# Kernel tuning notes

Hardware: AMD Instinct MI355X
Metric: run time of the kernel (lower is better)

The kernel has to match this reference:

```python
import jax, jax.numpy as jnp
import numpy as np

N = 50000      # nodes
E = 800000     # edges (avg degree 16)
DIN = 128
DH = 128
DOUT = 40
ALPHA = 0.1
BETA = 1.0


def gcn_conv(x, src, dst, ew, W, b, n):
    """PyG GCNConv: add self-loops, symmetric deg^-1/2 normalization, gather-scatter."""
    idx = jnp.arange(n)
    s = jnp.concatenate([src, idx])
    d = jnp.concatenate([dst, idx])
    w = jnp.concatenate([ew, jnp.ones((n,), x.dtype)])
    deg = jax.ops.segment_sum(w, d, num_segments=n)            # [N]
    dinv = jnp.where(deg > 0, jax.lax.rsqrt(deg), 0.0)
    norm = dinv[s] * w * dinv[d]                               # [E+N]
    h = x @ W                                                  # [N, dout]
    msg = h[s] * norm[:, None]                                 # gather + scale
    out = jax.ops.segment_sum(msg, d, num_segments=n)          # scatter-add
    return out + b


def setup_inputs() -> dict:
    key = jax.random.key(0)
    ks = jax.random.split(key, 10)
    x = jax.random.normal(ks[0], (N, DIN), jnp.float32)
    edge_index = jax.random.randint(ks[1], (2, E), 0, N, dtype=jnp.int64)
    edge_weight = jax.random.uniform(ks[2], (E,), jnp.float32)
    W1 = jax.random.normal(ks[3], (DIN, DH), jnp.float32) / np.float32(np.sqrt(DIN))
    b1 = jnp.zeros((DH,), jnp.float32)
    W2 = jax.random.normal(ks[4], (DH, DH), jnp.float32) / np.float32(np.sqrt(DH))
    b2 = jnp.zeros((DH,), jnp.float32)
    W3 = jax.random.normal(ks[5], (DH, DOUT), jnp.float32) / np.float32(np.sqrt(DH))
    b3 = jnp.zeros((DOUT,), jnp.float32)
    return {"x": x, "edge_index": edge_index, "edge_weight": edge_weight,
            "W1": W1, "b1": b1, "W2": W2, "b2": b2, "W3": W3, "b3": b3}


def reference(x, edge_index, edge_weight, W1, b1, W2, b2, W3, b3):
    src, dst = edge_index[0], edge_index[1]
    ones_w = jnp.ones((E,), x.dtype)
    h1 = jax.nn.relu(gcn_conv(x, src, dst, ones_w, W1, b1, N))   # conv1 (edge_weight=None)
    hc = gcn_conv(h1, src, dst, edge_weight, W2, b2, N)          # crf_layer with edge_weight
    h = ALPHA * h1 + BETA * hc                                   # weighted residual combo
    # LearnableBernoulliDropout: identity in eval mode
    out = gcn_conv(h, src, dst, ones_w, W3, b3, N)               # conv2
    return jax.nn.log_softmax(out, axis=1)
```

## Files before the change

### kernel.cpp

```cpp
#include <hip/hip_runtime.h>
#include <math.h>

#define DIN  128
#define DH   128
#define DOUT 40
#define ALPHA_C 0.1f
#define BETA_C  1.0f
#define SLOT 64

#define NPB 512
#define NPB_SHIFT 9
#define MAXBK 128
#define BCAP 12288

typedef __attribute__((ext_vector_type(8))) short short8;
typedef __attribute__((ext_vector_type(4))) float floatx4;

static inline int cdiv_h(int a, int b) { return (a + b - 1) / b; }

static __device__ __forceinline__ unsigned short f2b(float f) {
    unsigned u = __float_as_uint(f);
    u = u + 0x7FFFu + ((u >> 16) & 1u);
    return (unsigned short)(u >> 16);
}
static __device__ __forceinline__ unsigned pk2(float x, float y) {
    return (unsigned)f2b(x) | ((unsigned)f2b(y) << 16);
}
static __device__ __forceinline__ float2 b2f2(unsigned u) {
    float2 r;
    r.x = __uint_as_float(u << 16);
    r.y = __uint_as_float(u & 0xFFFF0000u);
    return r;
}
static __device__ __forceinline__ float b2f1(unsigned short u) {
    return __uint_as_float(((unsigned)u) << 16);
}

__global__ __launch_bounds__(256) void init_gcur(int* __restrict__ gcur, int nbk) {
    int b = threadIdx.x;
    if (b < nbk) gcur[b] = b * BCAP;
}

__global__ __launch_bounds__(256) void bucket_p1(const int* __restrict__ src,
                                                 const int* __restrict__ dst,
                                                 const float* __restrict__ ew,
                                                 int* __restrict__ gcur,
                                                 int2* __restrict__ stage,
                                                 int E, int nbk) {
    __shared__ int hist[MAXBK], off[MAXBK], sbase[MAXBK];
    int t = threadIdx.x;
    int nb = gridDim.x;
    int C = (E + nb - 1) / nb;
    int e0 = blockIdx.x * C;
    int e1 = e0 + C; if (e1 > E) e1 = E;

    for (int i = t; i < nbk; i += 256) { hist[i] = 0; off[i] = 0; }
    __syncthreads();
    for (int e = e0 + t; e < e1; e += 256)
        atomicAdd(&hist[dst[e] >> NPB_SHIFT], 1);
    __syncthreads();
    for (int i = t; i < nbk; i += 256)
        sbase[i] = atomicAdd(&gcur[i], hist[i]);
    __syncthreads();
    for (int e = e0 + t; e < e1; e += 256) {
        int d = dst[e];
        int b = d >> NPB_SHIFT;
        int pos = atomicAdd(&off[b], 1);
        int idx = sbase[b] + pos;
        if (idx < (b + 1) * BCAP) {
            int2 v;
            v.x = (src[e] & 0xFFFF) | ((d & (NPB - 1)) << 16);
            v.y = __float_as_int(ew[e]);
            stage[idx] = v;
        }
    }
}

__global__ __launch_bounds__(256) void bucket_p2(const int2* __restrict__ stage,
                                                 const int* __restrict__ gcur,
                                                 int2* __restrict__ csr,
                                                 int* __restrict__ cnt,
                                                 float* __restrict__ dinv1,
                                                 float* __restrict__ dinv2, int Nn) {
    __shared__ int   lcnt[NPB];
    __shared__ float lws[NPB];
    int b = blockIdx.x;
    int t = threadIdx.x;
    for (int i = t; i < NPB; i += 256) { lcnt[i] = 0; lws[i] = 0.f; }
    __syncthreads();

    int base = b * BCAP;
    int n = gcur[b] - base; if (n > BCAP) n = BCAP;
    for (int i = t; i < n; i += 256) {
        int2 v = stage[base + i];
        int dl = (v.x >> 16) & (NPB - 1);
        int pos = atomicAdd(&lcnt[dl], 1);
        atomicAdd(&lws[dl], __int_as_float(v.y));
        if (pos < SLOT) {
            int d = (b << NPB_SHIFT) + dl;
            int2 o; o.x = v.x & 0xFFFF; o.y = v.y;
            csr[(d << 6) + pos] = o;
        }
    }
    __syncthreads();

    int d0 = b << NPB_SHIFT;
    for (int i = t; i < NPB; i += 256) {
        int d = d0 + i;
        if (d < Nn) {
            int c = lcnt[i]; if (c > SLOT) c = SLOT;
            cnt[d] = c;
            dinv1[d] = rsqrtf((float)c + 1.f);
            dinv2[d] = rsqrtf(1.f + lws[i]);
        }
    }
}

template <bool ABF16>
__global__ __launch_bounds__(256) void gemm128(const void* __restrict__ Ain,
                                               const float* __restrict__ W,
                                               unsigned short* __restrict__ C, int M) {
    __shared__ short As[128 * 128];
    __shared__ short Bs[128 * 128];
    int t = threadIdx.x;
    int blockM = blockIdx.x * 128;

    {
        int r = t >> 1, h = t & 1;
        int rg = blockM + r; if (rg > M - 1) rg = M - 1;
        if (ABF16) {
            const uint4* arow = (const uint4*)((const unsigned short*)Ain + (size_t)rg * 128);
            #pragma unroll
            for (int i = 0; i < 8; ++i) {
                int chunk = h * 8 + i;
                uint4 v = arow[chunk];
                *(uint4*)&As[r * 128 + ((chunk ^ (r & 7)) * 8)] = v;
            }
        } else {
            const float4* arow = (const float4*)((const float*)Ain + (size_t)rg * 128);
            #pragma unroll
            for (int i = 0; i < 8; ++i) {
                int chunk = h * 8 + i;
                float4 v0 = arow[chunk * 2], v1 = arow[chunk * 2 + 1];
                uint4 p;
                p.x = pk2(v0.x, v0.y); p.y = pk2(v0.z, v0.w);
                p.z = pk2(v1.x, v1.y); p.w = pk2(v1.z, v1.w);
                *(uint4*)&As[r * 128 + ((chunk ^ (r & 7)) * 8)] = p;
            }
        }
    }
    {
        int n = t & 127;
        int k0 = (t >> 7) * 64;
        #pragma unroll
        for (int it = 0; it < 8; ++it) {
            int k = k0 + it * 8;
            float f0 = W[(size_t)(k + 0) * 128 + n];
            float f1 = W[(size_t)(k + 1) * 128 + n];
            float f2 = W[(size_t)(k + 2) * 128 + n];
            float f3 = W[(size_t)(k + 3) * 128 + n];
            float f4 = W[(size_t)(k + 4) * 128 + n];
            float f5 = W[(size_t)(k + 5) * 128 + n];
            float f6 = W[(size_t)(k + 6) * 128 + n];
            float f7 = W[(size_t)(k + 7) * 128 + n];
            uint4 p;
            p.x = pk2(f0, f1); p.y = pk2(f2, f3);
            p.z = pk2(f4, f5); p.w = pk2(f6, f7);
            *(uint4*)&Bs[n * 128 + (((k >> 3) ^ (n & 7)) * 8)] = p;
        }
    }
    __syncthreads();

    int w = t >> 6, l = t & 63;
    int q = l >> 4, lm = l & 15;
    int rowoff = (w >> 1) * 64, coloff = (w & 1) * 64;

    floatx4 acc[4][4] = {};
    #pragma unroll
    for (int ks = 0; ks < 4; ++ks) {
        int chunk = ks * 4 + q;
        int sw = (chunk ^ (lm & 7)) * 8;
        short8 af[4], bf[4];
        #pragma unroll
        for (int tm = 0; tm < 4; ++tm)
            af[tm] = *(const short8*)&As[(rowoff + tm * 16 + lm) * 128 + sw];
        #pragma unroll
        for (int tn = 0; tn < 4; ++tn)
            bf[tn] = *(const short8*)&Bs[(coloff + tn * 16 + lm) * 128 + sw];
        #pragma unroll
        for (int tm = 0; tm < 4; ++tm)
            #pragma unroll
            for (int tn = 0; tn < 4; ++tn)
                acc[tm][tn] = __builtin_amdgcn_mfma_f32_16x16x32_bf16(af[tm], bf[tn], acc[tm][tn], 0, 0, 0);
    }

    #pragma unroll
    for (int tm = 0; tm < 4; ++tm) {
        #pragma unroll
        for (int reg = 0; reg < 4; ++reg) {
            int row = blockM + rowoff + tm * 16 + q * 4 + reg;
            if (row >= M) continue;
            #pragma unroll
            for (int tn = 0; tn < 4; ++tn) {
                int col = coloff + tn * 16 + lm;
                C[(size_t)row * 128 + col] = f2b(acc[tm][tn][reg]);
            }
        }
    }
}

__global__ __launch_bounds__(256) void gemm40(const unsigned short* __restrict__ Ain,
                                              const float* __restrict__ W,
                                              unsigned short* __restrict__ Cb, int M) {
    __shared__ short As[128 * 128];
    __shared__ short Bs[48 * 128];
    int t = threadIdx.x;
    int blockM = blockIdx.x * 128;

    {
        int r = t >> 1, h = t & 1;
        int rg = blockM + r; if (rg > M - 1) rg = M - 1;
        const uint4* arow = (const uint4*)(Ain + (size_t)rg * 128);
        #pragma unroll
        for (int i = 0; i < 8; ++i) {
            int chunk = h * 8 + i;
            uint4 v = arow[chunk];
            *(uint4*)&As[r * 128 + ((chunk ^ (r & 7)) * 8)] = v;
        }
    }
    {
        int n = t & 63;
        int k0 = (t >> 6) * 32;
        #pragma unroll
        for (int it = 0; it < 4; ++it) {
            int k = k0 + it * 8;
            uint4 p = {0, 0, 0, 0};
            if (n < 40) {
                float f0 = W[(size_t)(k + 0) * 40 + n];
                float f1 = W[(size_t)(k + 1) * 40 + n];
                float f2 = W[(size_t)(k + 2) * 40 + n];
                float f3 = W[(size_t)(k + 3) * 40 + n];
                float f4 = W[(size_t)(k + 4) * 40 + n];
                float f5 = W[(size_t)(k + 5) * 40 + n];
                float f6 = W[(size_t)(k + 6) * 40 + n];
                float f7 = W[(size_t)(k + 7) * 40 + n];
                p.x = pk2(f0, f1); p.y = pk2(f2, f3);
                p.z = pk2(f4, f5); p.w = pk2(f6, f7);
            }
            if (n < 48)
                *(uint4*)&Bs[n * 128 + (((k >> 3) ^ (n & 7)) * 8)] = p;
        }
    }
    __syncthreads();

    int w = t >> 6, l = t & 63;
    int q = l >> 4, lm = l & 15;
    int rowoff = w * 32;

    floatx4 acc[2][3] = {};
    #pragma unroll
    for (int ks = 0; ks < 4; ++ks) {
        int chunk = ks * 4 + q;
        int sw = (chunk ^ (lm & 7)) * 8;
        short8 af[2], bf[3];
        #pragma unroll
        for (int tm = 0; tm < 2; ++tm)
            af[tm] = *(const short8*)&As[(rowoff + tm * 16 + lm) * 128 + sw];
        #pragma unroll
        for (int tn = 0; tn < 3; ++tn)
            bf[tn] = *(const short8*)&Bs[(tn * 16 + lm) * 128 + sw];
        #pragma unroll
        for (int tm = 0; tm < 2; ++tm)
            #pragma unroll
            for (int tn = 0; tn < 3; ++tn)
                acc[tm][tn] = __builtin_amdgcn_mfma_f32_16x16x32_bf16(af[tm], bf[tn], acc[tm][tn], 0, 0, 0);
    }

    #pragma unroll
    for (int tm = 0; tm < 2; ++tm) {
        #pragma unroll
        for (int reg = 0; reg < 4; ++reg) {
            int row = blockM + rowoff + tm * 16 + q * 4 + reg;
            if (row >= M) continue;
            Cb[(size_t)row * 40 + lm]      = f2b(acc[tm][0][reg]);
            Cb[(size_t)row * 40 + 16 + lm] = f2b(acc[tm][1][reg]);
            if (lm < 8)
                Cb[(size_t)row * 40 + 32 + lm] = f2b(acc[tm][2][reg]);
        }
    }
}

template <int MODE>
__global__ __launch_bounds__(256) void agg128(const unsigned short* __restrict__ hpre,
                                              unsigned short* __restrict__ io,
                                              const float* __restrict__ bias,
                                              const float* __restrict__ dinv,
                                              const int* __restrict__ cnt,
                                              const int2* __restrict__ csr, int n) {
    int row = blockIdx.x * 4 + (threadIdx.x >> 6);
    if (row >= n) return;
    int lane = threadIdx.x & 63;
    const unsigned* hp = (const unsigned*)hpre;

    float di = dinv[row];
    float d2 = di * di;
    float2 acc = b2f2(hp[(size_t)row * 64 + lane]);
    {
        float2 bb = ((const float2*)bias)[lane];
        acc.x = fmaf(acc.x, d2, bb.x);
        acc.y = fmaf(acc.y, d2, bb.y);
    }

    int c = cnt[row]; if (c > SLOT) c = SLOT;
    int jb = row << 6;
    int je = jb + c;
    int j = jb;

    while (j + 8 <= je) {
        int2 ee[8]; float2 ff[8];
        #pragma unroll
        for (int u = 0; u < 8; ++u) ee[u] = csr[j + u];
        #pragma unroll
        for (int u = 0; u < 8; ++u) ff[u] = b2f2(hp[(size_t)ee[u].x * 64 + lane]);
        #pragma unroll
        for (int u = 0; u < 8; ++u) {
            float cc = (MODE == 1) ? dinv[ee[u].x] * __int_as_float(ee[u].y) * di
                                   : dinv[ee[u].x] * di;
            acc.x = fmaf(cc, ff[u].x, acc.x);
            acc.y = fmaf(cc, ff[u].y, acc.y);
        }
        j += 8;
    }
    if (j + 4 <= je) {
        int2 ee[4]; float2 ff[4];
        #pragma unroll
        for (int u = 0; u < 4; ++u) ee[u] = csr[j + u];
        #pragma unroll
        for (int u = 0; u < 4; ++u) ff[u] = b2f2(hp[(size_t)ee[u].x * 64 + lane]);
        #pragma unroll
        for (int u = 0; u < 4; ++u) {
            float cc = (MODE == 1) ? dinv[ee[u].x] * __int_as_float(ee[u].y) * di
                                   : dinv[ee[u].x] * di;
            acc.x = fmaf(cc, ff[u].x, acc.x);
            acc.y = fmaf(cc, ff[u].y, acc.y);
        }
        j += 4;
    }
    for (; j < je; ++j) {
        int2 e0 = csr[j];
        float cc = (MODE == 1) ? dinv[e0.x] * __int_as_float(e0.y) * di
                               : dinv[e0.x] * di;
        float2 f0 = b2f2(hp[(size_t)e0.x * 64 + lane]);
        acc.x = fmaf(cc, f0.x, acc.x);
        acc.y = fmaf(cc, f0.y, acc.y);
    }

    unsigned* iop = (unsigned*)io;
    if (MODE == 0) {
        acc.x = fmaxf(acc.x, 0.f); acc.y = fmaxf(acc.y, 0.f);
        iop[(size_t)row * 64 + lane] = pk2(acc.x, acc.y);
    } else {
        float2 h1 = b2f2(iop[(size_t)row * 64 + lane]);
        acc.x = fmaf(ALPHA_C, h1.x, BETA_C * acc.x);
        acc.y = fmaf(ALPHA_C, h1.y, BETA_C * acc.y);
        iop[(size_t)row * 64 + lane] = pk2(acc.x, acc.y);
    }
}

__global__ __launch_bounds__(256) void agg40_lsm(const unsigned short* __restrict__ h40,
                                                 const float* __restrict__ bias,
                                                 const float* __restrict__ dinv,
                                                 const int* __restrict__ cnt,
                                                 const int2* __restrict__ csr,
                                                 float* __restrict__ out, int n) {
    int row = blockIdx.x * 4 + (threadIdx.x >> 6);
    if (row >= n) return;
    int lane = threadIdx.x & 63;
    bool act = lane < 40;
    int ln = act ? lane : 39;

    float di = dinv[row];
    float d2 = di * di;
    float acc = b2f1(h40[(size_t)row * 40 + ln]) * d2;

    int c = cnt[row]; if (c > SLOT) c = SLOT;
    int jb = row << 6;
    int je = jb + c;
    int j = jb;

    while (j + 8 <= je) {
        int ss[8]; float ff[8];
        #pragma unroll
        for (int u = 0; u < 8; ++u) ss[u] = csr[j + u].x;
        #pragma unroll
        for (int u = 0; u < 8; ++u) ff[u] = b2f1(h40[(size_t)ss[u] * 40 + ln]);
        #pragma unroll
        for (int u = 0; u < 8; ++u)
            acc = fmaf(dinv[ss[u]] * di, ff[u], acc);
        j += 8;
    }
    if (j + 4 <= je) {
        int ss[4]; float ff[4];
        #pragma unroll
        for (int u = 0; u < 4; ++u) ss[u] = csr[j + u].x;
        #pragma unroll
        for (int u = 0; u < 4; ++u) ff[u] = b2f1(h40[(size_t)ss[u] * 40 + ln]);
        #pragma unroll
        for (int u = 0; u < 4; ++u)
            acc = fmaf(dinv[ss[u]] * di, ff[u], acc);
        j += 4;
    }
    for (; j < je; ++j) {
        int s0 = csr[j].x;
        acc = fmaf(dinv[s0] * di, b2f1(h40[(size_t)s0 * 40 + ln]), acc);
    }

    float v = act ? (acc + bias[ln]) : -INFINITY;
    float mx = v;
    #pragma unroll
    for (int o = 1; o < 64; o <<= 1) mx = fmaxf(mx, __shfl_xor(mx, o, 64));
    float e = act ? expf(v - mx) : 0.f;
    float ssum = e;
    #pragma unroll
    for (int o = 1; o < 64; o <<= 1) ssum += __shfl_xor(ssum, o, 64);
    float ls = mx + logf(ssum);
    if (act) out[(size_t)row * 40 + lane] = v - ls;
}

extern "C" void kernel_launch(void* const* d_in, const int* in_sizes, int n_in,
                              void* d_out, int out_size, void* d_ws, size_t ws_size,
                              hipStream_t stream) {
    const float* x   = (const float*)d_in[0];
    const int*   ei  = (const int*)  d_in[1];
    const float* ew  = (const float*)d_in[2];
    const float* W1  = (const float*)d_in[3];
    const float* b1  = (const float*)d_in[4];
    const float* W2  = (const float*)d_in[5];
    const float* b2  = (const float*)d_in[6];
    const float* W3  = (const float*)d_in[7];
    const float* b3  = (const float*)d_in[8];
    float* out = (float*)d_out;

    const int Nn = in_sizes[0] / DIN;
    const int E  = in_sizes[1] / 2;
    const int* src = ei;
    const int* dst = ei + E;

    char* wsb = (char*)d_ws;
    int*   cnt     = (int*)wsb;                          wsb += (size_t)Nn * 4;
    float* dinv1   = (float*)wsb;                        wsb += (size_t)Nn * 4;
    float* dinv2   = (float*)wsb;                        wsb += (size_t)Nn * 4;
    int2*  csr     = (int2*)wsb;                         wsb += (size_t)Nn * SLOT * 8;
    unsigned short* hpreb = (unsigned short*)wsb;        wsb += (size_t)Nn * DH * 2;
    unsigned short* h1b   = (unsigned short*)wsb;        wsb += (size_t)Nn * DH * 2;
    int*   gcur    = (int*)wsb;                          wsb += (size_t)MAXBK * 4;

    int2* stage = (int2*)hpreb;
    int nbk = cdiv_h(Nn, NPB);

    init_gcur<<<1, 256, 0, stream>>>(gcur, nbk);
    bucket_p1<<<128, 256, 0, stream>>>(src, dst, ew, gcur, stage, E, nbk);
    bucket_p2<<<nbk, 256, 0, stream>>>(stage, gcur, csr, cnt, dinv1, dinv2, Nn);

    int gemmGrid = cdiv_h(Nn, 128);
    int aggGrid = cdiv_h(Nn, 4);

    gemm128<false><<<gemmGrid, 256, 0, stream>>>(x, W1, hpreb, Nn);
    agg128<0><<<aggGrid, 256, 0, stream>>>(hpreb, h1b, b1, dinv1, cnt, csr, Nn);

    gemm128<true><<<gemmGrid, 256, 0, stream>>>(h1b, W2, hpreb, Nn);
    agg128<1><<<aggGrid, 256, 0, stream>>>(hpreb, h1b, b2, dinv2, cnt, csr, Nn);

    unsigned short* h40 = hpreb;
    gemm40<<<gemmGrid, 256, 0, stream>>>(h1b, W3, h40, Nn);
    agg40_lsm<<<aggGrid, 256, 0, stream>>>(h40, b3, dinv1, cnt, csr, out, Nn);
}
```

Baseline: 272.8 us.

## Split 128-wide aggregation into feature slices with edge-parallel lanes

Replaces the per-row wavefront aggregation, where each lane owns two features and loops over all edges, with a sliced scheme. Each block handles one of four 32-feature slices for four rows. The 64 lanes split into 4 edge groups of 16 lanes, and partial sums are combined with cross-lane shuffles. This raises the number of independent gathers in flight per wave and multiplies the grid by four to expose more parallelism for the memory-latency-bound gather. In exchange, each gather segment is only 64 bytes, and the CSR indices and dinv values are reloaded once per slice.

```diff
diff --git a/kernel.cpp b/kernel.cpp
--- a/kernel.cpp
+++ b/kernel.cpp
@@ -12,6 +12,8 @@
 #define NPB_SHIFT 9
 #define MAXBK 128
 #define BCAP 12288
+
+#define SLICES 4
 
 typedef __attribute__((ext_vector_type(8))) short short8;
 typedef __attribute__((ext_vector_type(4))) float floatx4;
@@ -291,79 +293,77 @@
 }
 
 template <int MODE>
-__global__ __launch_bounds__(256) void agg128(const unsigned short* __restrict__ hpre,
-                                              unsigned short* __restrict__ io,
-                                              const float* __restrict__ bias,
-                                              const float* __restrict__ dinv,
-                                              const int* __restrict__ cnt,
-                                              const int2* __restrict__ csr, int n) {
-    int row = blockIdx.x * 4 + (threadIdx.x >> 6);
+__global__ __launch_bounds__(256) void agg_slice(const unsigned short* __restrict__ hpre,
+                                                 unsigned short* __restrict__ io,
+                                                 const float* __restrict__ bias,
+                                                 const float* __restrict__ dinv,
+                                                 const int* __restrict__ cnt,
+                                                 const int2* __restrict__ csr, int n) {
+    int bid = blockIdx.x;
+    int slice = bid & (SLICES - 1);
+    int row = (bid >> 2) * 4 + (threadIdx.x >> 6);
     if (row >= n) return;
     int lane = threadIdx.x & 63;
+    int eg = lane >> 4, ci = lane & 15;
+    int soff = slice * 16 + ci;
     const unsigned* hp = (const unsigned*)hpre;
 
     float di = dinv[row];
-    float d2 = di * di;
-    float2 acc = b2f2(hp[(size_t)row * 64 + lane]);
-    {
-        float2 bb = ((const float2*)bias)[lane];
-        acc.x = fmaf(acc.x, d2, bb.x);
-        acc.y = fmaf(acc.y, d2, bb.y);
-    }
+    float2 acc = {0.f, 0.f};
 
     int c = cnt[row]; if (c > SLOT) c = SLOT;
     int jb = row << 6;
-    int je = jb + c;
-    int j = jb;
-
-    while (j + 8 <= je) {
-        int2 ee[8]; float2 ff[8];
-        #pragma unroll
-        for (int u = 0; u < 8; ++u) ee[u] = csr[j + u];
-        #pragma unroll
-        for (int u = 0; u < 8; ++u) ff[u] = b2f2(hp[(size_t)ee[u].x * 64 + lane]);
-        #pragma unroll
-        for (int u = 0; u < 8; ++u) {
-            float cc = (MODE == 1) ? dinv[ee[u].x] * __int_as_float(ee[u].y) * di
-                                   : dinv[ee[u].x] * di;
-            acc.x = fmaf(cc, ff[u].x, acc.x);
-            acc.y = fmaf(cc, ff[u].y, acc.y);
-        }
-        j += 8;
-    }
-    if (j + 4 <= je) {
-        int2 ee[4]; float2 ff[4];
-        #pragma unroll
-        for (int u = 0; u < 4; ++u) ee[u] = csr[j + u];
-        #pragma unroll
-        for (int u = 0; u < 4; ++u) ff[u] = b2f2(hp[(size_t)ee[u].x * 64 + lane]);
-        #pragma unroll
-        for (int u = 0; u < 4; ++u) {
-            float cc = (MODE == 1) ? dinv[ee[u].x] * __int_as_float(ee[u].y) * di
-                                   : dinv[ee[u].x] * di;
-            acc.x = fmaf(cc, ff[u].x, acc.x);
-            acc.y = fmaf(cc, ff[u].y, acc.y);
-        }
-        j += 4;
-    }
-    for (; j < je; ++j) {
-        int2 e0 = csr[j];
-        float cc = (MODE == 1) ? dinv[e0.x] * __int_as_float(e0.y) * di
-                               : dinv[e0.x] * di;
-        float2 f0 = b2f2(hp[(size_t)e0.x * 64 + lane]);
-        acc.x = fmaf(cc, f0.x, acc.x);
-        acc.y = fmaf(cc, f0.y, acc.y);
-    }
-
-    unsigned* iop = (unsigned*)io;
-    if (MODE == 0) {
-        acc.x = fmaxf(acc.x, 0.f); acc.y = fmaxf(acc.y, 0.f);
-        iop[(size_t)row * 64 + lane] = pk2(acc.x, acc.y);
-    } else {
-        float2 h1 = b2f2(iop[(size_t)row * 64 + lane]);
-        acc.x = fmaf(ALPHA_C, h1.x, BETA_C * acc.x);
-        acc.y = fmaf(ALPHA_C, h1.y, BETA_C * acc.y);
-        iop[(size_t)row * 64 + lane] = pk2(acc.x, acc.y);
+    int k = 0;
+    while (k + 8 <= c) {
+        int2 eA = csr[jb + k + eg];
+        int2 eB = csr[jb + k + 4 + eg];
+        unsigned fA = hp[(size_t)eA.x * 64 + soff];
+        unsigned fB = hp[(size_t)eB.x * 64 + soff];
+        float cA = (MODE == 1) ? dinv[eA.x] * __int_as_float(eA.y) * di : dinv[eA.x] * di;
+        float cB = (MODE == 1) ? dinv[eB.x] * __int_as_float(eB.y) * di : dinv[eB.x] * di;
+        float2 a = b2f2(fA), b = b2f2(fB);
+        acc.x = fmaf(cA, a.x, acc.x); acc.y = fmaf(cA, a.y, acc.y);
+        acc.x = fmaf(cB, b.x, acc.x); acc.y = fmaf(cB, b.y, acc.y);
+        k += 8;
+    }
+    if (k + 4 <= c) {
+        int2 eA = csr[jb + k + eg];
+        unsigned fA = hp[(size_t)eA.x * 64 + soff];
+        float cA = (MODE == 1) ? dinv[eA.x] * __int_as_float(eA.y) * di : dinv[eA.x] * di;
+        float2 a = b2f2(fA);
+        acc.x = fmaf(cA, a.x, acc.x); acc.y = fmaf(cA, a.y, acc.y);
+        k += 4;
+    }
+    if (k < c) {
+        int idx = k + eg;
+        int2 eA = csr[jb + ((idx < c) ? idx : (c - 1))];
+        float valid = (idx < c) ? 1.f : 0.f;
+        unsigned fA = hp[(size_t)eA.x * 64 + soff];
+        float cA = ((MODE == 1) ? dinv[eA.x] * __int_as_float(eA.y) * di : dinv[eA.x] * di) * valid;
+        float2 a = b2f2(fA);
+        acc.x = fmaf(cA, a.x, acc.x); acc.y = fmaf(cA, a.y, acc.y);
+    }
+
+    acc.x += __shfl_xor(acc.x, 16, 64); acc.y += __shfl_xor(acc.y, 16, 64);
+    acc.x += __shfl_xor(acc.x, 32, 64); acc.y += __shfl_xor(acc.y, 32, 64);
+
+    if (eg == 0) {
+        float d2 = di * di;
+        float2 s = b2f2(hp[(size_t)row * 64 + soff]);
+        float2 bb = ((const float2*)bias)[soff];
+        acc.x = fmaf(s.x, d2, acc.x) + bb.x;
+        acc.y = fmaf(s.y, d2, acc.y) + bb.y;
+        unsigned* iop = (unsigned*)io;
+        size_t o = (size_t)row * 64 + soff;
+        if (MODE == 0) {
+            acc.x = fmaxf(acc.x, 0.f); acc.y = fmaxf(acc.y, 0.f);
+            iop[o] = pk2(acc.x, acc.y);
+        } else {
+            float2 h1 = b2f2(iop[o]);
+            acc.x = fmaf(ALPHA_C, h1.x, BETA_C * acc.x);
+            acc.y = fmaf(ALPHA_C, h1.y, BETA_C * acc.y);
+            iop[o] = pk2(acc.x, acc.y);
+        }
     }
 }
 
@@ -463,13 +463,14 @@
     bucket_p2<<<nbk, 256, 0, stream>>>(stage, gcur, csr, cnt, dinv1, dinv2, Nn);
 
     int gemmGrid = cdiv_h(Nn, 128);
-    int aggGrid = cdiv_h(Nn, 4);
+    int aggGrid  = cdiv_h(Nn, 4);
+    int sliceGrid = aggGrid * SLICES;
 
     gemm128<false><<<gemmGrid, 256, 0, stream>>>(x, W1, hpreb, Nn);
-    agg128<0><<<aggGrid, 256, 0, stream>>>(hpreb, h1b, b1, dinv1, cnt, csr, Nn);
+    agg_slice<0><<<sliceGrid, 256, 0, stream>>>(hpreb, h1b, b1, dinv1, cnt, csr, Nn);
 
     gemm128<true><<<gemmGrid, 256, 0, stream>>>(h1b, W2, hpreb, Nn);
-    agg128<1><<<aggGrid, 256, 0, stream>>>(hpreb, h1b, b2, dinv2, cnt, csr, Nn);
+    agg_slice<1><<<sliceGrid, 256, 0, stream>>>(hpreb, h1b, b2, dinv2, cnt, csr, Nn);
 
     unsigned short* h40 = hpreb;
     gemm40<<<gemmGrid, 256, 0, stream>>>(h1b, W3, h40, Nn);
```

New measurement: 360.7 us. +32.2%, slower.
